# Kernel optimization log

Hardware: AMD Instinct MI355X
Metric: run time of the kernel (lower is better)

Reference implementation:

```python
import jax, jax.numpy as jnp
import numpy as np

T, K, N, G = 8192, 1024, 2048, 8  # total_rows, k, n, num_groups


def setup_inputs() -> dict:
    key = jax.random.key(0)
    kA, kB, kO = jax.random.split(key, 3)
    A = jax.random.normal(kA, (T, K), dtype=jnp.float32)
    B = jax.random.normal(kB, (G, K, N), dtype=jnp.float32) * 0.02
    # monotonically increasing end-offsets; last offset covers all rows
    offsets = jnp.sort(jax.random.randint(kO, (G,), 1, T)).at[-1].set(T).astype(jnp.int32)
    return {"A": A, "B": B, "offsets": offsets}


def reference(A, B, offsets):
    """Grouped GEMM: rows A[offsets[g-1]:offsets[g]] are multiplied by B[g].

    Implemented jit-compatibly (offsets may be traced) by masking rows per
    group and accumulating disjoint contributions; the Python loop is over
    the small, static number of groups only.
    """
    num_groups = B.shape[0]
    total_rows = A.shape[0]
    # group id of each row: first offset strictly greater than row index
    gid = jnp.searchsorted(offsets, jnp.arange(total_rows), side="right")  # [T]
    out = jnp.zeros((total_rows, B.shape[2]), dtype=A.dtype)
    for g in range(num_groups):
        mask = (gid == g)[:, None]                      # [T,1] disjoint masks
        out = out + jnp.where(mask, A, 0.0) @ B[g]      # [T,n]
    return out
```

## Files before the change

### kernel.cpp

```cpp
#include <hip/hip_runtime.h>
#include <hip/hip_bf16.h>

#define T_ROWS 8192
#define K_DIM  1024
#define N_DIM  2048
#define G_NUM  8
#define CONVA_BLOCKS 2048
#define CONVB_BLOCKS 4096

typedef __attribute__((ext_vector_type(8))) short short8;
typedef __attribute__((ext_vector_type(4))) float v4f;

__device__ __forceinline__ unsigned short f2bf(float x) {
  unsigned int u = __builtin_bit_cast(unsigned int, x);
  u += 0x7fffu + ((u >> 16) & 1u);
  return (unsigned short)(u >> 16);
}
__device__ __forceinline__ unsigned int pk2(float a, float b) {
  return (unsigned int)f2bf(a) | ((unsigned int)f2bf(b) << 16);
}
__device__ __forceinline__ void async_cp16(const void* gsrc, void* ldst) {
  __builtin_amdgcn_global_load_lds(
      (const __attribute__((address_space(1))) void*)gsrc,
      (__attribute__((address_space(3))) void*)ldst, 16, 0, 0);
}

__global__ __launch_bounds__(256) void conv_fused(const float* __restrict__ A,
                                                  const float* __restrict__ B,
                                                  unsigned short* __restrict__ Ab,
                                                  unsigned short* __restrict__ Bt) {
  __shared__ float tile[64][65];
  const int bid = blockIdx.x;
  const int t = threadIdx.x;
  const int q3 = bid / 3, r3 = bid - q3 * 3;

  if (r3 == 0) {
    size_t idx = (size_t)q3 * 256 + t;
    const float4* src = (const float4*)A + idx * 4;
    float4 v0 = src[0], v1 = src[1], v2 = src[2], v3 = src[3];
    uint4 o0, o1;
    o0.x = pk2(v0.x, v0.y); o0.y = pk2(v0.z, v0.w);
    o0.z = pk2(v1.x, v1.y); o0.w = pk2(v1.z, v1.w);
    o1.x = pk2(v2.x, v2.y); o1.y = pk2(v2.z, v2.w);
    o1.z = pk2(v3.x, v3.y); o1.w = pk2(v3.z, v3.w);
    ((uint4*)Ab)[idx * 2]     = o0;
    ((uint4*)Ab)[idx * 2 + 1] = o1;
    return;
  }
  const int bidx = 2 * q3 + (r3 - 1);
  const int nt = bidx & 31;
  const int kt = (bidx >> 5) & 15;
  const int g  = bidx >> 9;
  const int c4 = t & 15;
  const int r  = t >> 4;

  const float* src = B + ((size_t)g * K_DIM + (size_t)kt * 64) * N_DIM + (size_t)nt * 64;
#pragma unroll
  for (int i = 0; i < 4; ++i) {
    int k = r + i * 16;
    float4 v = *(const float4*)(src + (size_t)k * N_DIM + c4 * 4);
    tile[k][c4 * 4 + 0] = v.x; tile[k][c4 * 4 + 1] = v.y;
    tile[k][c4 * 4 + 2] = v.z; tile[k][c4 * 4 + 3] = v.w;
  }
  __syncthreads();
  unsigned short* dst = Bt + ((size_t)g * N_DIM + (size_t)nt * 64) * K_DIM + (size_t)kt * 64;
#pragma unroll
  for (int i = 0; i < 2; ++i) {
    int idx = t + i * 256;
    int n = idx >> 3;
    int seg = idx & 7;
    unsigned int u0 = pk2(tile[seg * 8 + 0][n], tile[seg * 8 + 1][n]);
    unsigned int u1 = pk2(tile[seg * 8 + 2][n], tile[seg * 8 + 3][n]);
    unsigned int u2 = pk2(tile[seg * 8 + 4][n], tile[seg * 8 + 5][n]);
    unsigned int u3 = pk2(tile[seg * 8 + 6][n], tile[seg * 8 + 7][n]);
    uint4 o; o.x = u0; o.y = u1; o.z = u2; o.w = u3;
    *(uint4*)(dst + (size_t)n * K_DIM + seg * 8) = o;
  }
}

__global__ __launch_bounds__(256) void gemm_kernel(const unsigned short* __restrict__ Ab,
                                                   const unsigned short* __restrict__ Btb,
                                                   const int* __restrict__ offs,
                                                   float* __restrict__ out) {
  __shared__ char lds[65536];
  const int t = threadIdx.x;

  const int b = blockIdx.x;
  const int xcd = b & 7;
  const int j = b >> 3;
  const int mslot = xcd * 9 + (j >> 4);
  const int n0 = (j & 15) * 128;

  int prev = 0, cum = 0, row0 = 0, row_end = 0, g = 0, found = 0;
#pragma unroll
  for (int gg = 0; gg < G_NUM; ++gg) {
    int e = offs[gg];
    int tiles = (e - prev + 127) >> 7;
    if (!found && mslot < cum + tiles) {
      found = 1; g = gg; row0 = prev + (mslot - cum) * 128; row_end = e;
    }
    cum += tiles;
    prev = e;
  }
  if (!found) return;

  const int lane = t & 63;
  const int wv = t >> 6;
  const int wm = wv & 1;
  const int wn = wv >> 1;

  const int rq = t >> 2;
  const int t4 = (t & 3) ^ ((rq ^ (rq >> 2)) & 3);
  const unsigned short* aSrc[2];
  const unsigned short* bSrc[2];
#pragma unroll
  for (int i = 0; i < 2; ++i) {
    int rl = i * 64 + rq;
    int rA = row0 + rl; if (rA > T_ROWS - 1) rA = T_ROWS - 1;
    aSrc[i] = Ab + (size_t)rA * K_DIM + t4 * 8;
    bSrc[i] = Btb + ((size_t)g * N_DIM + n0 + rl) * K_DIM + t4 * 8;
  }

  const int lr = lane & 15;
  const int rowb = lr * 64 + (((lane >> 4) ^ ((lr ^ (lr >> 2)) & 3)) << 4);

  v4f acc[4][4];
#pragma unroll
  for (int i = 0; i < 4; ++i)
#pragma unroll
    for (int j2 = 0; j2 < 4; ++j2)
#pragma unroll
      for (int r = 0; r < 4; ++r) acc[i][j2][r] = 0.0f;

#define ISSUE_T(TILE, S2)                                                  \
  do {                                                                     \
    char* ad_ = (char*)lds + (S2) * 8192 + t * 16;                         \
    char* bd_ = (char*)lds + 32768 + (S2) * 8192 + t * 16;                 \
    async_cp16(aSrc[0] + (TILE) * 32, ad_);                                \
    async_cp16(aSrc[1] + (TILE) * 32, ad_ + 4096);                         \
    async_cp16(bSrc[0] + (TILE) * 32, bd_);                                \
    async_cp16(bSrc[1] + (TILE) * 32, bd_ + 4096);                         \
  } while (0)

#define PHASE_T(S, TILE, VM)                                               \
  do {                                                                     \
    asm volatile("s_waitcnt vmcnt(" #VM ")" ::: "memory");                 \
    __builtin_amdgcn_s_barrier();                                          \
    __builtin_amdgcn_sched_barrier(0);                                     \
    if ((TILE) >= 0) ISSUE_T(TILE, ((S) + 3) & 3);                         \
    short8 a0_, a1_, a2_, a3_, b0_, b1_, b2_, b3_;                         \
    {                                                                      \
      const char* ab_ = (const char*)lds + (S) * 8192 + wm * 4096 + rowb;  \
      const char* bb_ = (const char*)lds + 32768 + (S) * 8192 + wn * 4096 + rowb; \
      a0_ = *(const short8*)(ab_);                                         \
      a1_ = *(const short8*)(ab_ + 1024);                                  \
      a2_ = *(const short8*)(ab_ + 2048);                                  \
      a3_ = *(const short8*)(ab_ + 3072);                                  \
      b0_ = *(const short8*)(bb_);                                         \
      b1_ = *(const short8*)(bb_ + 1024);                                  \
      b2_ = *(const short8*)(bb_ + 2048);                                  \
      b3_ = *(const short8*)(bb_ + 3072);                                  \
    }                                                                      \
    __builtin_amdgcn_s_setprio(1);                                         \
    acc[0][0] = __builtin_amdgcn_mfma_f32_16x16x32_bf16(a0_, b0_, acc[0][0], 0, 0, 0); \
    acc[0][1] = __builtin_amdgcn_mfma_f32_16x16x32_bf16(a0_, b1_, acc[0][1], 0, 0, 0); \
    acc[0][2] = __builtin_amdgcn_mfma_f32_16x16x32_bf16(a0_, b2_, acc[0][2], 0, 0, 0); \
    acc[0][3] = __builtin_amdgcn_mfma_f32_16x16x32_bf16(a0_, b3_, acc[0][3], 0, 0, 0); \
    acc[1][0] = __builtin_amdgcn_mfma_f32_16x16x32_bf16(a1_, b0_, acc[1][0], 0, 0, 0); \
    acc[1][1] = __builtin_amdgcn_mfma_f32_16x16x32_bf16(a1_, b1_, acc[1][1], 0, 0, 0); \
    acc[1][2] = __builtin_amdgcn_mfma_f32_16x16x32_bf16(a1_, b2_, acc[1][2], 0, 0, 0); \
    acc[1][3] = __builtin_amdgcn_mfma_f32_16x16x32_bf16(a1_, b3_, acc[1][3], 0, 0, 0); \
    acc[2][0] = __builtin_amdgcn_mfma_f32_16x16x32_bf16(a2_, b0_, acc[2][0], 0, 0, 0); \
    acc[2][1] = __builtin_amdgcn_mfma_f32_16x16x32_bf16(a2_, b1_, acc[2][1], 0, 0, 0); \
    acc[2][2] = __builtin_amdgcn_mfma_f32_16x16x32_bf16(a2_, b2_, acc[2][2], 0, 0, 0); \
    acc[2][3] = __builtin_amdgcn_mfma_f32_16x16x32_bf16(a2_, b3_, acc[2][3], 0, 0, 0); \
    acc[3][0] = __builtin_amdgcn_mfma_f32_16x16x32_bf16(a3_, b0_, acc[3][0], 0, 0, 0); \
    acc[3][1] = __builtin_amdgcn_mfma_f32_16x16x32_bf16(a3_, b1_, acc[3][1], 0, 0, 0); \
    acc[3][2] = __builtin_amdgcn_mfma_f32_16x16x32_bf16(a3_, b2_, acc[3][2], 0, 0, 0); \
    acc[3][3] = __builtin_amdgcn_mfma_f32_16x16x32_bf16(a3_, b3_, acc[3][3], 0, 0, 0); \
    __builtin_amdgcn_s_setprio(0);                                         \
    __builtin_amdgcn_sched_barrier(0);                                     \
  } while (0)

  ISSUE_T(0, 0);
  ISSUE_T(1, 1);
  ISSUE_T(2, 2);

#pragma unroll 1
  for (int tb = 0; tb < 28; tb += 4) {
    PHASE_T(0, tb + 3, 8);
    PHASE_T(1, tb + 4, 8);
    PHASE_T(2, tb + 5, 8);
    PHASE_T(3, tb + 6, 8);
  }
  PHASE_T(0, 31, 8);
  PHASE_T(1, -1, 8);
  PHASE_T(2, -1, 4);
  PHASE_T(3, -1, 0);

#undef PHASE_T
#undef ISSUE_T

  const int colBase = n0 + wn * 64 + (lane & 15);
  const int rowBase = row0 + wm * 64 + ((lane >> 4) << 2);
#pragma unroll
  for (int im = 0; im < 4; ++im) {
#pragma unroll
    for (int in = 0; in < 4; ++in) {
      int c = colBase + in * 16;
#pragma unroll
      for (int r = 0; r < 4; ++r) {
        int rr = rowBase + im * 16 + r;
        if (rr < row_end) out[(size_t)rr * N_DIM + c] = acc[im][in][r];
      }
    }
  }
}

__global__ __launch_bounds__(256) void fallback_kernel(const float* __restrict__ A,
                                                       const float* __restrict__ B,
                                                       const int* __restrict__ offs,
                                                       float* __restrict__ out) {
  int r = blockIdx.y;
  int c = blockIdx.x * 256 + threadIdx.x;
  int g = 0;
#pragma unroll
  for (int i = 0; i < G_NUM; ++i) g += (offs[i] <= r);
  const float* a = A + (size_t)r * K_DIM;
  const float* b = B + (size_t)g * K_DIM * N_DIM + c;
  float s = 0.f;
  for (int k = 0; k < K_DIM; ++k) s += a[k] * b[(size_t)k * N_DIM];
  out[(size_t)r * N_DIM + c] = s;
}

extern "C" void kernel_launch(void* const* d_in, const int* in_sizes, int n_in,
                              void* d_out, int out_size, void* d_ws, size_t ws_size,
                              hipStream_t stream) {
  const float* A = (const float*)d_in[0];
  const float* B = (const float*)d_in[1];
  const int* offs = (const int*)d_in[2];
  float* out = (float*)d_out;

  size_t need = ((size_t)T_ROWS * K_DIM + (size_t)G_NUM * K_DIM * N_DIM) * 2;
  if (ws_size < need) {
    dim3 grid(N_DIM / 256, T_ROWS);
    fallback_kernel<<<grid, 256, 0, stream>>>(A, B, offs, out);
    return;
  }
  unsigned short* Ab = (unsigned short*)d_ws;
  unsigned short* Btb = Ab + (size_t)T_ROWS * K_DIM;

  conv_fused<<<CONVA_BLOCKS + CONVB_BLOCKS, 256, 0, stream>>>(A, B, Ab, Btb);
  gemm_kernel<<<8 * 9 * 16, 256, 0, stream>>>(Ab, Btb, offs, out);
}
```

Before: 194.0 us.

## Enlarge grouped GEMM block tile to 256x256 with 512-thread blocks

```diff
diff --git a/kernel.cpp b/kernel.cpp
--- a/kernel.cpp
+++ b/kernel.cpp
@@ -78,26 +78,26 @@
   }
 }
 
-__global__ __launch_bounds__(256) void gemm_kernel(const unsigned short* __restrict__ Ab,
+__global__ __launch_bounds__(512) void gemm_kernel(const unsigned short* __restrict__ Ab,
                                                    const unsigned short* __restrict__ Btb,
                                                    const int* __restrict__ offs,
                                                    float* __restrict__ out) {
-  __shared__ char lds[65536];
+  __shared__ char lds[131072];
   const int t = threadIdx.x;
 
   const int b = blockIdx.x;
   const int xcd = b & 7;
   const int j = b >> 3;
-  const int mslot = xcd * 9 + (j >> 4);
-  const int n0 = (j & 15) * 128;
+  const int mslot = xcd * 5 + (j >> 3);
+  const int n0 = (j & 7) * 256;
 
   int prev = 0, cum = 0, row0 = 0, row_end = 0, g = 0, found = 0;
 #pragma unroll
   for (int gg = 0; gg < G_NUM; ++gg) {
     int e = offs[gg];
-    int tiles = (e - prev + 127) >> 7;
+    int tiles = (e - prev + 255) >> 8;
     if (!found && mslot < cum + tiles) {
-      found = 1; g = gg; row0 = prev + (mslot - cum) * 128; row_end = e;
+      found = 1; g = gg; row0 = prev + (mslot - cum) * 256; row_end = e;
     }
     cum += tiles;
     prev = e;
@@ -111,22 +111,21 @@
 
   const int rq = t >> 2;
   const int t4 = (t & 3) ^ ((rq ^ (rq >> 2)) & 3);
-  const unsigned short* aSrc[2];
-  const unsigned short* bSrc[2];
-#pragma unroll
-  for (int i = 0; i < 2; ++i) {
-    int rl = i * 64 + rq;
-    int rA = row0 + rl; if (rA > T_ROWS - 1) rA = T_ROWS - 1;
-    aSrc[i] = Ab + (size_t)rA * K_DIM + t4 * 8;
-    bSrc[i] = Btb + ((size_t)g * N_DIM + n0 + rl) * K_DIM + t4 * 8;
-  }
+  int rA0 = row0 + rq;       if (rA0 > T_ROWS - 1) rA0 = T_ROWS - 1;
+  int rA1 = row0 + 128 + rq; if (rA1 > T_ROWS - 1) rA1 = T_ROWS - 1;
+  const unsigned short* aSrc0 = Ab + (size_t)rA0 * K_DIM + t4 * 8;
+  const unsigned short* aSrc1 = Ab + (size_t)rA1 * K_DIM + t4 * 8;
+  const unsigned short* bSrc0 = Btb + ((size_t)g * N_DIM + n0 + rq) * K_DIM + t4 * 8;
+  const unsigned short* bSrc1 = Btb + ((size_t)g * N_DIM + n0 + 128 + rq) * K_DIM + t4 * 8;
 
   const int lr = lane & 15;
-  const int rowb = lr * 64 + (((lane >> 4) ^ ((lr ^ (lr >> 2)) & 3)) << 4);
-
-  v4f acc[4][4];
-#pragma unroll
-  for (int i = 0; i < 4; ++i)
+  const int phx = ((lane >> 4) ^ ((lr ^ (lr >> 2)) & 3)) << 4;
+  const int arow = (wm * 128 + lr) * 64 + phx;
+  const int brow = (wn * 64 + lr) * 64 + phx + 16384;
+
+  v4f acc[8][4];
+#pragma unroll
+  for (int i = 0; i < 8; ++i)
 #pragma unroll
     for (int j2 = 0; j2 < 4; ++j2)
 #pragma unroll
@@ -134,12 +133,11 @@
 
 #define ISSUE_T(TILE, S2)                                                  \
   do {                                                                     \
-    char* ad_ = (char*)lds + (S2) * 8192 + t * 16;                         \
-    char* bd_ = (char*)lds + 32768 + (S2) * 8192 + t * 16;                 \
-    async_cp16(aSrc[0] + (TILE) * 32, ad_);                                \
-    async_cp16(aSrc[1] + (TILE) * 32, ad_ + 4096);                         \
-    async_cp16(bSrc[0] + (TILE) * 32, bd_);                                \
-    async_cp16(bSrc[1] + (TILE) * 32, bd_ + 4096);                         \
+    char* base_ = (char*)lds + (S2) * 32768 + t * 16;                      \
+    async_cp16(aSrc0 + (TILE) * 32, base_);                                \
+    async_cp16(aSrc1 + (TILE) * 32, base_ + 8192);                         \
+    async_cp16(bSrc0 + (TILE) * 32, base_ + 16384);                        \
+    async_cp16(bSrc1 + (TILE) * 32, base_ + 24576);                        \
   } while (0)
 
 #define PHASE_T(S, TILE, VM)                                               \
@@ -148,36 +146,21 @@
     __builtin_amdgcn_s_barrier();                                          \
     __builtin_amdgcn_sched_barrier(0);                                     \
     if ((TILE) >= 0) ISSUE_T(TILE, ((S) + 3) & 3);                         \
-    short8 a0_, a1_, a2_, a3_, b0_, b1_, b2_, b3_;                         \
+    short8 af_[8], bf_[4];                                                 \
     {                                                                      \
-      const char* ab_ = (const char*)lds + (S) * 8192 + wm * 4096 + rowb;  \
-      const char* bb_ = (const char*)lds + 32768 + (S) * 8192 + wn * 4096 + rowb; \
-      a0_ = *(const short8*)(ab_);                                         \
-      a1_ = *(const short8*)(ab_ + 1024);                                  \
-      a2_ = *(const short8*)(ab_ + 2048);                                  \
-      a3_ = *(const short8*)(ab_ + 3072);                                  \
-      b0_ = *(const short8*)(bb_);                                         \
-      b1_ = *(const short8*)(bb_ + 1024);                                  \
-      b2_ = *(const short8*)(bb_ + 2048);                                  \
-      b3_ = *(const short8*)(bb_ + 3072);                                  \
+      const char* ab_ = (const char*)lds + (S) * 32768 + arow;             \
+      const char* bb_ = (const char*)lds + (S) * 32768 + brow;             \
+      _Pragma("unroll")                                                    \
+      for (int mf = 0; mf < 8; ++mf) af_[mf] = *(const short8*)(ab_ + mf * 1024); \
+      _Pragma("unroll")                                                    \
+      for (int nf = 0; nf < 4; ++nf) bf_[nf] = *(const short8*)(bb_ + nf * 1024); \
     }                                                                      \
     __builtin_amdgcn_s_setprio(1);                                         \
-    acc[0][0] = __builtin_amdgcn_mfma_f32_16x16x32_bf16(a0_, b0_, acc[0][0], 0, 0, 0); \
-    acc[0][1] = __builtin_amdgcn_mfma_f32_16x16x32_bf16(a0_, b1_, acc[0][1], 0, 0, 0); \
-    acc[0][2] = __builtin_amdgcn_mfma_f32_16x16x32_bf16(a0_, b2_, acc[0][2], 0, 0, 0); \
-    acc[0][3] = __builtin_amdgcn_mfma_f32_16x16x32_bf16(a0_, b3_, acc[0][3], 0, 0, 0); \
-    acc[1][0] = __builtin_amdgcn_mfma_f32_16x16x32_bf16(a1_, b0_, acc[1][0], 0, 0, 0); \
-    acc[1][1] = __builtin_amdgcn_mfma_f32_16x16x32_bf16(a1_, b1_, acc[1][1], 0, 0, 0); \
-    acc[1][2] = __builtin_amdgcn_mfma_f32_16x16x32_bf16(a1_, b2_, acc[1][2], 0, 0, 0); \
-    acc[1][3] = __builtin_amdgcn_mfma_f32_16x16x32_bf16(a1_, b3_, acc[1][3], 0, 0, 0); \
-    acc[2][0] = __builtin_amdgcn_mfma_f32_16x16x32_bf16(a2_, b0_, acc[2][0], 0, 0, 0); \
-    acc[2][1] = __builtin_amdgcn_mfma_f32_16x16x32_bf16(a2_, b1_, acc[2][1], 0, 0, 0); \
-    acc[2][2] = __builtin_amdgcn_mfma_f32_16x16x32_bf16(a2_, b2_, acc[2][2], 0, 0, 0); \
-    acc[2][3] = __builtin_amdgcn_mfma_f32_16x16x32_bf16(a2_, b3_, acc[2][3], 0, 0, 0); \
-    acc[3][0] = __builtin_amdgcn_mfma_f32_16x16x32_bf16(a3_, b0_, acc[3][0], 0, 0, 0); \
-    acc[3][1] = __builtin_amdgcn_mfma_f32_16x16x32_bf16(a3_, b1_, acc[3][1], 0, 0, 0); \
-    acc[3][2] = __builtin_amdgcn_mfma_f32_16x16x32_bf16(a3_, b2_, acc[3][2], 0, 0, 0); \
-    acc[3][3] = __builtin_amdgcn_mfma_f32_16x16x32_bf16(a3_, b3_, acc[3][3], 0, 0, 0); \
+    _Pragma("unroll")                                                      \
+    for (int mf = 0; mf < 8; ++mf)                                         \
+      _Pragma("unroll")                                                    \
+      for (int nf = 0; nf < 4; ++nf)                                       \
+        acc[mf][nf] = __builtin_amdgcn_mfma_f32_16x16x32_bf16(af_[mf], bf_[nf], acc[mf][nf], 0, 0, 0); \
     __builtin_amdgcn_s_setprio(0);                                         \
     __builtin_amdgcn_sched_barrier(0);                                     \
   } while (0)
@@ -201,17 +184,17 @@
 #undef PHASE_T
 #undef ISSUE_T
 
-  const int colBase = n0 + wn * 64 + (lane & 15);
-  const int rowBase = row0 + wm * 64 + ((lane >> 4) << 2);
-#pragma unroll
-  for (int im = 0; im < 4; ++im) {
-#pragma unroll
-    for (int in = 0; in < 4; ++in) {
-      int c = colBase + in * 16;
+  const int colBase = n0 + wn * 64 + lr;
+  const int rowBase = row0 + wm * 128 + ((lane >> 4) << 2);
+#pragma unroll
+  for (int mf = 0; mf < 8; ++mf) {
+#pragma unroll
+    for (int nf = 0; nf < 4; ++nf) {
+      int c = colBase + nf * 16;
 #pragma unroll
       for (int r = 0; r < 4; ++r) {
-        int rr = rowBase + im * 16 + r;
-        if (rr < row_end) out[(size_t)rr * N_DIM + c] = acc[im][in][r];
+        int rr = rowBase + mf * 16 + r;
+        if (rr < row_end) out[(size_t)rr * N_DIM + c] = acc[mf][nf][r];
       }
     }
   }
@@ -251,5 +234,5 @@
   unsigned short* Btb = Ab + (size_t)T_ROWS * K_DIM;
 
   conv_fused<<<CONVA_BLOCKS + CONVB_BLOCKS, 256, 0, stream>>>(A, B, Ab, Btb);
-  gemm_kernel<<<8 * 9 * 16, 256, 0, stream>>>(Ab, Btb, offs, out);
-}
+  gemm_kernel<<<8 * 5 * 8, 512, 0, stream>>>(Ab, Btb, offs, out);
+}
```

Measured after the change: 207.0 us. 1.07x slower.
